# Performance work log

Hardware: AMD Instinct MI355X
Metric: run time of the kernel (lower is better)

## Reference

```python
import jax, jax.numpy as jnp
import numpy as np

X, U, AD, H = 32, 8, 24, 256
T, B = 128, 256
MIN_V, MAX_V = 0.01, 1.0
EPS = 1e-6


def setup_inputs() -> dict:
    key = jax.random.key(0)
    ks = jax.random.split(key, 10)
    s = lambda k, sh: jax.random.normal(k, sh, jnp.float32) * 0.05
    return {
        "u": jax.random.normal(ks[0], (T, B, U), jnp.float32),
        "a": jax.random.normal(ks[1], (T, B, AD), jnp.float32),
        "W1": s(ks[2], (H, X)), "b1": jnp.zeros((H,), jnp.float32),
        "W2": s(ks[3], (H, H)), "b2": jnp.zeros((H,), jnp.float32),
        "WA": s(ks[4], (X * X, H)), "bA": jnp.zeros((X * X,), jnp.float32),
        "WB": s(ks[5], (X * U, H)), "bB": jnp.zeros((X * U,), jnp.float32),
        "WC": s(ks[6], (AD * X, H)), "bC": jnp.zeros((AD * X,), jnp.float32),
        "Wnx": s(ks[7], (X, H)), "bnx": jnp.zeros((X,), jnp.float32),
        "Wna": s(ks[8], (AD, H)), "bna": jnp.zeros((AD,), jnp.float32),
        "alpha": jnp.array([0.01], jnp.float32),
    }


def _forward(u, a, W1, b1, W2, b2, WA, bA, WB, bB, WC, bC, Wnx, bnx, Wna, bna, alpha):
    eyeX = jnp.eye(X, dtype=u.dtype)
    eyeA = jnp.eye(AD, dtype=u.dtype)

    def dyn(x):
        # locally-linear dynamics heads; x: [B, X]
        h = jax.nn.relu(x @ W1.T + b1)
        h = jax.nn.relu(h @ W2.T + b2)
        b = x.shape[0]
        Am = eyeX + alpha[0] * (h @ WA.T + bA).reshape(b, X, X)
        Bm = (h @ WB.T + bB).reshape(b, X, U)
        Cm = (h @ WC.T + bC).reshape(b, AD, X)
        nx = MIN_V + (MAX_V - MIN_V) * jax.nn.sigmoid(h @ Wnx.T + bnx)
        na = MIN_V + (MAX_V - MIN_V) * jax.nn.sigmoid(h @ Wna.T + bna)
        return Am, Bm, Cm, nx, na

    def make_psd(P):
        return 0.5 * (P + jnp.swapaxes(P, -1, -2)) + EPS * eyeX

    def prior_step(mean, cov, u_t):
        Am, Bm, _, nx, _ = dyn(mean)
        nm = jnp.einsum('bij,bj->bi', Am, mean) + jnp.einsum('bij,bj->bi', Bm, u_t)
        nc = jnp.einsum('bij,bjk,blk->bil', Am, cov, Am) + nx[:, :, None] * eyeX
        return nm, make_psd(nc)

    def post_step(mean, cov, a_t):
        _, _, Cm, _, na = dyn(mean)
        S = jnp.einsum('bij,bjk,blk->bil', Cm, cov, Cm) + na[:, :, None] * eyeA
        Sp = jnp.linalg.pinv(S)
        G = jnp.einsum('bij,bkj,bkl->bil', cov, Cm, Sp)  # cov @ C^T @ pinv(S)
        innov = a_t - jnp.einsum('bij,bj->bi', Cm, mean)
        nm = mean + jnp.einsum('bij,bj->bi', G, innov)
        nc = cov - jnp.einsum('bij,bjk,bkl->bil', G, Cm, cov)
        return nm, make_psd(nc)

    pm0 = jnp.zeros((B, X), u.dtype)
    pc0 = jnp.broadcast_to(eyeX, (B, X, X))
    qm0, qc0 = post_step(pm0, pc0, a[0])

    def step(carry, inp):
        qm, qc = carry
        u_t, a_next = inp
        prm, prc = prior_step(qm, qc, u_t)
        nqm, nqc = post_step(prm, prc, a_next)
        return (nqm, nqc), (prm, prc, nqm, nqc)

    _, (prm, prc, qm, qc) = jax.lax.scan(step, (qm0, qc0), (u[:-1], a[1:]))
    prior_means = jnp.concatenate([pm0[None], prm], axis=0)
    prior_covs = jnp.concatenate([pc0[None], prc], axis=0)
    post_means = jnp.concatenate([qm0[None], qm], axis=0)
    post_covs = jnp.concatenate([qc0[None], qc], axis=0)
    return prior_means, prior_covs, post_means, post_covs


def reference(u, a, W1, b1, W2, b2, WA, bA, WB, bB, WC, bC, Wnx, bnx, Wna, bna, alpha):
    return _forward(u, a, W1, b1, W2, b2, WA, bA, WB, bB, WC, bC, Wnx, bnx, Wna, bna, alpha)
```

## Files before the change

kernel.cpp:

```cpp
#include <hip/hip_runtime.h>
#include <hip/hip_bf16.h>
#include <math.h>

typedef unsigned int uint32;
typedef _Float16 h2_t __attribute__((ext_vector_type(2)));

static constexpr int NX = 32;
static constexpr int NU = 8;
static constexpr int NA = 24;
static constexpr int NH = 256;
static constexpr int NT = 128;
static constexpr int NB = 256;
static constexpr float MINV = 0.01f, MAXV = 1.0f, EPSV = 1e-6f;

static constexpr int H1O = NX*NX + NX*NU + NX;
static constexpr int H1P = 1344;
static constexpr int H2O = NA*NX + NA;
static constexpr int H2P = 800;

static constexpr size_t OFF_W1 = 0;
static constexpr size_t OFF_W2 = 4096;
static constexpr size_t OFF_H1 = OFF_W2 + 32768;
static constexpr size_t OFF_H2 = OFF_H1 + 172032;
static constexpr size_t OFF_B1 = OFF_H2 + 102400;
static constexpr size_t OFF_B2 = OFF_B1 + 1344;

__global__ void pack_half_off(const float* __restrict__ src, uint32* __restrict__ dst,
                              int O, int K, int LDP, int off)
{
    int idx = blockIdx.x * blockDim.x + threadIdx.x;
    int K2 = K >> 1;
    if (idx >= O * K2) return;
    int kk = idx % K2;
    int o  = idx / K2;
    int k  = kk * 2;
    int k8 = k >> 3, q = (k >> 1) & 3;
    _Float16 a = (_Float16)src[o * K + k];
    _Float16 b = (_Float16)src[o * K + k + 1];
    uint32 val = (uint32)__builtin_bit_cast(unsigned short, a)
               | ((uint32)__builtin_bit_cast(unsigned short, b) << 16);
    dst[((size_t)k8 * LDP + off + o) * 4 + q] = val;
}

__global__ void pack_bias3(const float* __restrict__ s0, int n0,
                           const float* __restrict__ s1, int n1,
                           const float* __restrict__ s2, int n2,
                           float* __restrict__ dst)
{
    int i = blockIdx.x * blockDim.x + threadIdx.x;
    if (i < n0) dst[i] = s0[i];
    else if (i < n0 + n1) dst[i] = s1[i - n0];
    else if (i < n0 + n1 + n2) dst[i] = s2[i - n0 - n1];
}

__device__ __forceinline__ float dot2(uint32 w, uint32 x, float acc)
{
#if __has_builtin(__builtin_amdgcn_fdot2)
    return __builtin_amdgcn_fdot2(__builtin_bit_cast(h2_t, w),
                                  __builtin_bit_cast(h2_t, x), acc, false);
#else
    h2_t a = __builtin_bit_cast(h2_t, w), b = __builtin_bit_cast(h2_t, x);
    return acc + (float)a[0] * (float)b[0] + (float)a[1] * (float)b[1];
#endif
}

__device__ __forceinline__ float dot8(uint4 w, uint4 x, float acc)
{
    acc = dot2(w.x, x.x, acc);
    acc = dot2(w.y, x.y, acc);
    acc = dot2(w.z, x.z, acc);
    acc = dot2(w.w, x.w, acc);
    return acc;
}

__device__ __forceinline__ void tri_decode(int p, int& l, int& i)
{
    int lo = (int)((sqrtf(8.f * (float)p + 1.f) - 1.f) * 0.5f);
    while ((lo + 1) * (lo + 2) / 2 <= p) lo++;
    while (lo * (lo + 1) / 2 > p) lo--;
    l = lo;
    i = p - lo * (lo + 1) / 2;
}

__device__ __forceinline__ float sigm_scaled(float z)
{
    return MINV + (MAXV - MINV) / (1.f + expf(-z));
}

__device__ __forceinline__ unsigned short f2h(float v)
{
    _Float16 h = (_Float16)v;
    return __builtin_bit_cast(unsigned short, h);
}

__global__ __launch_bounds__(512) void kf_kernel(
    const float* __restrict__ u, const float* __restrict__ a,
    const uint32* __restrict__ wsu,
    const float* __restrict__ b1, const float* __restrict__ b2,
    const float* __restrict__ alpha_p,
    float* __restrict__ out)
{
    const int tid = threadIdx.x;
    const int b   = blockIdx.x;
    const float alpha = alpha_p[0];

    const uint4* W1h = (const uint4*)(wsu + OFF_W1);
    const uint4* W2h = (const uint4*)(wsu + OFF_W2);
    const uint4* H1h = (const uint4*)(wsu + OFF_H1);
    const uint4* H2h = (const uint4*)(wsu + OFF_H2);
    const float* BH1 = (const float*)(wsu + OFF_B1);
    const float* BH2 = (const float*)(wsu + OFF_B2);

    __shared__ alignas(16) uint32 s_h1h[NH / 2];
    __shared__ alignas(16) uint32 s_h2h[NH / 2];
    __shared__ alignas(16) uint32 s_qmh[NX / 2];
    __shared__ alignas(16) uint32 s_pmh[NX / 2];
    __shared__ float s_part[2][NH];
    __shared__ float s_Am[NX * NX];
    __shared__ float s_Bm[NX * NU];
    __shared__ float s_nx[NX];
    __shared__ float s_C[NA * NX];
    __shared__ float s_na[NA];
    __shared__ float s_qm[NX], s_qc[NX * NX];
    __shared__ float s_pm[NX], s_pc[NX * NX];
    __shared__ float s_T2[NX * NX];
    __shared__ float s_T1[NA * NX];
    __shared__ float s_S[NA * NA];
    __shared__ float s_Y[NA * NX];
    __shared__ float s_innov[NA];
    __shared__ float s_a[NA], s_u[NU];

    const size_t pmO = 0;
    const size_t pcO = (size_t)NT * NB * NX;
    const size_t qmO = pcO + (size_t)NT * NB * NX * NX;
    const size_t qcO = qmO + (size_t)NT * NB * NX;

    for (int t = 0; t < NT; ++t) {
        const size_t mIdx = (size_t)t * NB + b;

        if (t == 0) {
            if (tid < NX) s_pm[tid] = 0.f;
            if (tid < NX / 2) s_pmh[tid] = 0u;
            {
                int o = tid;           s_pc[o] = ((o >> 5) == (o & 31)) ? 1.f : 0.f;
                o = tid + 512;         s_pc[o] = ((o >> 5) == (o & 31)) ? 1.f : 0.f;
            }
            __syncthreads();
        } else {
            if (tid < NH) {
                const uint4* xh = (const uint4*)s_qmh;
                float acc = b1[tid];
                #pragma unroll
                for (int k8 = 0; k8 < 4; k8++)
                    acc = dot8(W1h[k8 * NH + tid], xh[k8], acc);
                float v = fmaxf(acc, 0.f);
                unsigned short us = f2h(v);
                int pi = __shfl_xor((int)us, 1);
                if ((tid & 1) == 0)
                    s_h1h[tid >> 1] = (uint32)us | ((uint32)pi << 16);
            } else {
                const size_t mPrev = (size_t)(t - 1) * NB + b;
                for (int s = tid - 256; s < NX + NX * NX; s += 256) {
                    if (s < NX)
                        __builtin_nontemporal_store(s_qm[s], out + qmO + mPrev * NX + s);
                    else
                        __builtin_nontemporal_store(s_qc[s - NX], out + qcO + mPrev * NX * NX + (s - NX));
                }
                if (tid - 256 < NU)
                    s_u[tid - 256] = u[((size_t)(t - 1) * NB + b) * NU + (tid - 256)];
            }
            __syncthreads();

            {
                int o = tid & 255, g = tid >> 8;
                const uint4* xh = (const uint4*)s_h1h;
                float acc = 0.f;
                #pragma unroll 4
                for (int k8 = g * 16; k8 < g * 16 + 16; k8++)
                    acc = dot8(W2h[k8 * NH + o], xh[k8], acc);
                s_part[g][o] = acc;
            }
            __syncthreads();

            if (tid < NH) {
                float v = fmaxf(s_part[0][tid] + s_part[1][tid] + b2[tid], 0.f);
                unsigned short us = f2h(v);
                int pi = __shfl_xor((int)us, 1);
                if ((tid & 1) == 0)
                    s_h2h[tid >> 1] = (uint32)us | ((uint32)pi << 16);
            }
            __syncthreads();

            {
                const uint4* xh = (const uint4*)s_h2h;
                int o0 = tid, o1 = tid + 512, o2 = tid + 1024;
                float a0 = BH1[o0], a1 = BH1[o1];
                float a2 = (tid < 320) ? BH1[o2] : 0.f;
                #pragma unroll 4
                for (int k8 = 0; k8 < 32; k8++) {
                    uint4 x = xh[k8];
                    a0 = dot8(H1h[k8 * H1P + o0], x, a0);
                    a1 = dot8(H1h[k8 * H1P + o1], x, a1);
                    if (tid < 320) a2 = dot8(H1h[k8 * H1P + o2], x, a2);
                }
                #pragma unroll
                for (int r = 0; r < 3; r++) {
                    int o = (r == 0) ? o0 : (r == 1) ? o1 : o2;
                    float acc = (r == 0) ? a0 : (r == 1) ? a1 : a2;
                    if (r == 2 && tid >= 320) break;
                    if (o < NX * NX) {
                        s_Am[o] = (((o >> 5) == (o & 31)) ? 1.f : 0.f) + alpha * acc;
                    } else if (o < NX * NX + NX * NU) {
                        s_Bm[o - NX * NX] = acc;
                    } else if (o < H1O) {
                        s_nx[o - (NX * NX + NX * NU)] = sigm_scaled(acc);
                    }
                }
            }
            __syncthreads();

            #pragma unroll
            for (int r = 0; r < 2; r++) {
                int o = tid + 512 * r, i = o >> 5, l = o & 31;
                float acc = 0.f;
                #pragma unroll
                for (int j = 0; j < NX; j++)
                    acc = fmaf(s_Am[i * NX + j], s_qc[j * NX + l], acc);
                s_T2[o] = acc;
            }
            if (tid < NX) {
                float acc = 0.f;
                #pragma unroll
                for (int j = 0; j < NX; j++) acc = fmaf(s_Am[tid * NX + j], s_qm[j], acc);
                #pragma unroll
                for (int j = 0; j < NU; j++) acc = fmaf(s_Bm[tid * NU + j], s_u[j], acc);
                s_pm[tid] = acc;
                unsigned short us = f2h(acc);
                int pi = __shfl_xor((int)us, 1);
                if ((tid & 1) == 0)
                    s_pmh[tid >> 1] = (uint32)us | ((uint32)pi << 16);
            }
            __syncthreads();

            for (int p = tid; p < NX * (NX + 1) / 2; p += 512) {
                int l, i; tri_decode(p, l, i);
                float a_il = 0.f, a_li = 0.f;
                #pragma unroll
                for (int j = 0; j < NX; j++) {
                    a_il = fmaf(s_T2[i * NX + j], s_Am[l * NX + j], a_il);
                    a_li = fmaf(s_T2[l * NX + j], s_Am[i * NX + j], a_li);
                }
                if (i == l) {
                    s_pc[i * NX + i] = a_il + s_nx[i] + EPSV;
                } else {
                    float v = 0.5f * (a_il + a_li);
                    s_pc[i * NX + l] = v;
                    s_pc[l * NX + i] = v;
                }
            }
            __syncthreads();
        }

        if (tid < NH) {
            const uint4* xh = (const uint4*)s_pmh;
            float acc = b1[tid];
            #pragma unroll
            for (int k8 = 0; k8 < 4; k8++)
                acc = dot8(W1h[k8 * NH + tid], xh[k8], acc);
            float v = fmaxf(acc, 0.f);
            unsigned short us = f2h(v);
            int pi = __shfl_xor((int)us, 1);
            if ((tid & 1) == 0)
                s_h1h[tid >> 1] = (uint32)us | ((uint32)pi << 16);
        } else {
            for (int s = tid - 256; s < NX + NX * NX; s += 256) {
                if (s < NX)
                    __builtin_nontemporal_store(s_pm[s], out + pmO + mIdx * NX + s);
                else
                    __builtin_nontemporal_store(s_pc[s - NX], out + pcO + mIdx * NX * NX + (s - NX));
            }
            if (tid - 256 < NA)
                s_a[tid - 256] = a[mIdx * NA + (tid - 256)];
        }
        __syncthreads();

        {
            int o = tid & 255, g = tid >> 8;
            const uint4* xh = (const uint4*)s_h1h;
            float acc = 0.f;
            #pragma unroll 4
            for (int k8 = g * 16; k8 < g * 16 + 16; k8++)
                acc = dot8(W2h[k8 * NH + o], xh[k8], acc);
            s_part[g][o] = acc;
        }
        __syncthreads();

        if (tid < NH) {
            float v = fmaxf(s_part[0][tid] + s_part[1][tid] + b2[tid], 0.f);
            unsigned short us = f2h(v);
            int pi = __shfl_xor((int)us, 1);
            if ((tid & 1) == 0)
                s_h2h[tid >> 1] = (uint32)us | ((uint32)pi << 16);
        }
        __syncthreads();

        {
            const uint4* xh = (const uint4*)s_h2h;
            int o0 = tid, o1 = tid + 512;
            float a0 = BH2[o0];
            float a1 = (tid < H2P - 512) ? BH2[o1] : 0.f;
            #pragma unroll 4
            for (int k8 = 0; k8 < 32; k8++) {
                uint4 x = xh[k8];
                a0 = dot8(H2h[k8 * H2P + o0], x, a0);
                if (tid < H2P - 512) a1 = dot8(H2h[k8 * H2P + o1], x, a1);
            }
            if (o0 < NA * NX) s_C[o0] = a0;
            else if (o0 < H2O) s_na[o0 - NA * NX] = sigm_scaled(a0);
            if (tid < H2P - 512) {
                if (o1 < NA * NX) s_C[o1] = a1;
                else if (o1 < H2O) s_na[o1 - NA * NX] = sigm_scaled(a1);
            }
        }
        __syncthreads();

        {
            int p = tid;
            if (p < NA * NX) {
                int i = p >> 5, l = p & 31;
                float acc = 0.f;
                #pragma unroll
                for (int k = 0; k < NX; k++)
                    acc = fmaf(s_C[i * NX + k], s_pc[k * NX + l], acc);
                s_T1[p] = acc;
            }
            int p2 = tid + 512;
            if (p2 < NA * NX) {
                int i = p2 >> 5, l = p2 & 31;
                float acc = 0.f;
                #pragma unroll
                for (int k = 0; k < NX; k++)
                    acc = fmaf(s_C[i * NX + k], s_pc[k * NX + l], acc);
                s_T1[p2] = acc;
            }
            if (tid >= 488) {
                int i = tid - 488;
                float acc = s_a[i];
                #pragma unroll
                for (int j = 0; j < NX; j++)
                    acc = fmaf(-s_C[i * NX + j], s_pm[j], acc);
                s_innov[i] = acc;
            }
        }
        __syncthreads();

        if (tid < NA * (NA + 1) / 2) {
            int l, i; tri_decode(tid, l, i);
            float acc = 0.f;
            #pragma unroll
            for (int j = 0; j < NX; j++)
                acc = fmaf(s_T1[i * NX + j], s_C[l * NX + j], acc);
            if (i == l) acc += s_na[i];
            s_S[i * NA + l] = acc;
            s_S[l * NA + i] = acc;
        }
        __syncthreads();

        if (tid < 64) {
            const int j = tid;
            float r[NA];
            #pragma unroll
            for (int i = 0; i < NA; i++) {
                float v = 0.f;
                if (j < NA) v = s_S[i * NA + j];
                else if (j < NA + NX) v = s_T1[i * NX + (j - NA)];
                r[i] = v;
            }
            #pragma unroll
            for (int k = 0; k < NA; k++) {
                float piv = __shfl(r[k], k);
                float ip = 1.0f / piv;
                r[k] *= ip;
                #pragma unroll
                for (int i = 0; i < NA; i++) {
                    if (i == k) continue;
                    float f = __shfl(r[i], k);
                    r[i] = fmaf(-f, r[k], r[i]);
                }
            }
            if (j >= NA && j < NA + NX) {
                #pragma unroll
                for (int i = 0; i < NA; i++) s_Y[i * NX + (j - NA)] = r[i];
            }
        }
        __syncthreads();

        if (tid < NX) {
            float acc = s_pm[tid];
            #pragma unroll
            for (int i = 0; i < NA; i++)
                acc = fmaf(s_Y[i * NX + tid], s_innov[i], acc);
            s_qm[tid] = acc;
            unsigned short us = f2h(acc);
            int pi = __shfl_xor((int)us, 1);
            if ((tid & 1) == 0)
                s_qmh[tid >> 1] = (uint32)us | ((uint32)pi << 16);
        }
        for (int p = tid; p < NX * (NX + 1) / 2; p += 512) {
            int l, i; tri_decode(p, l, i);
            float t_il = 0.f, t_li = 0.f;
            #pragma unroll
            for (int q = 0; q < NA; q++) {
                t_il = fmaf(s_Y[q * NX + i], s_T1[q * NX + l], t_il);
                t_li = fmaf(s_Y[q * NX + l], s_T1[q * NX + i], t_li);
            }
            if (i == l) {
                s_qc[i * NX + i] = s_pc[i * NX + i] - t_il + EPSV;
            } else {
                float v = 0.5f * ((s_pc[i * NX + l] - t_il) + (s_pc[l * NX + i] - t_li));
                s_qc[i * NX + l] = v;
                s_qc[l * NX + i] = v;
            }
        }
        __syncthreads();
    }

    {
        const size_t mLast = (size_t)(NT - 1) * NB + b;
        for (int s = tid; s < NX + NX * NX; s += 512) {
            if (s < NX)
                __builtin_nontemporal_store(s_qm[s], out + qmO + mLast * NX + s);
            else
                __builtin_nontemporal_store(s_qc[s - NX], out + qcO + mLast * NX * NX + (s - NX));
        }
    }
}

extern "C" void kernel_launch(void* const* d_in, const int* in_sizes, int n_in,
                              void* d_out, int out_size, void* d_ws, size_t ws_size,
                              hipStream_t stream)
{
    const float* u    = (const float*)d_in[0];
    const float* a    = (const float*)d_in[1];
    const float* W1   = (const float*)d_in[2];
    const float* b1   = (const float*)d_in[3];
    const float* W2   = (const float*)d_in[4];
    const float* b2   = (const float*)d_in[5];
    const float* WA   = (const float*)d_in[6];
    const float* bA   = (const float*)d_in[7];
    const float* WB   = (const float*)d_in[8];
    const float* bB   = (const float*)d_in[9];
    const float* WC   = (const float*)d_in[10];
    const float* bC   = (const float*)d_in[11];
    const float* Wnx  = (const float*)d_in[12];
    const float* bnx  = (const float*)d_in[13];
    const float* Wna  = (const float*)d_in[14];
    const float* bna  = (const float*)d_in[15];
    const float* alph = (const float*)d_in[16];

    uint32* wsu = (uint32*)d_ws;
    float* out = (float*)d_out;

    auto pk = [&](const float* src, int O, int K, size_t dst_off, int LDP, int off) {
        int n = O * (K / 2);
        pack_half_off<<<(n + 255) / 256, 256, 0, stream>>>(src, wsu + dst_off, O, K, LDP, off);
    };
    pk(W1,  NH,      NX, OFF_W1, NH,  0);
    pk(W2,  NH,      NH, OFF_W2, NH,  0);
    pk(WA,  NX * NX, NH, OFF_H1, H1P, 0);
    pk(WB,  NX * NU, NH, OFF_H1, H1P, NX * NX);
    pk(Wnx, NX,      NH, OFF_H1, H1P, NX * NX + NX * NU);
    pk(WC,  NA * NX, NH, OFF_H2, H2P, 0);
    pk(Wna, NA,      NH, OFF_H2, H2P, NA * NX);

    pack_bias3<<<(H1O + 255) / 256, 256, 0, stream>>>(bA, NX * NX, bB, NX * NU, bnx, NX,
                                                      (float*)(wsu + OFF_B1));
    pack_bias3<<<(H2O + 255) / 256, 256, 0, stream>>>(bC, NA * NX, bna, NA, nullptr, 0,
                                                      (float*)(wsu + OFF_B2));

    kf_kernel<<<NB, 512, 0, stream>>>(u, a, wsu, b1, b2, alph, out);
}
```

Baseline: 4.138 ms.

## Process two batch elements per block to reuse weight loads and pad shared matrices

Each block now runs the Kalman filter recurrence for two batch elements instead of one, so every fp16 weight vector loaded from global memory is used in two dot products. Shared-memory matrices are padded to a row stride of 33 to cut bank conflicts. The grid halves to 128 blocks, which on a 256-CU device leaves half the CUs idle and lengthens each block's per-step serial work. Shared-memory use also roughly doubles.

```diff
diff --git a/kernel.cpp b/kernel.cpp
--- a/kernel.cpp
+++ b/kernel.cpp
@@ -11,6 +11,7 @@
 static constexpr int NH = 256;
 static constexpr int NT = 128;
 static constexpr int NB = 256;
+static constexpr int NXP = NX + 1;
 static constexpr float MINV = 0.01f, MAXV = 1.0f, EPSV = 1e-6f;
 
 static constexpr int H1O = NX*NX + NX*NU + NX;
@@ -93,6 +94,18 @@
     return __builtin_bit_cast(unsigned short, h);
 }
 
+__device__ __forceinline__ void pack2_to(int tid, float v0, float v1,
+                                         uint32* d0, uint32* d1)
+{
+    unsigned short u0 = f2h(v0), u1 = f2h(v1);
+    int p0 = __shfl_xor((int)u0, 1);
+    int p1 = __shfl_xor((int)u1, 1);
+    if ((tid & 1) == 0) {
+        d0[tid >> 1] = (uint32)u0 | ((uint32)p0 << 16);
+        d1[tid >> 1] = (uint32)u1 | ((uint32)p1 << 16);
+    }
+}
+
 __global__ __launch_bounds__(512) void kf_kernel(
     const float* __restrict__ u, const float* __restrict__ a,
     const uint32* __restrict__ wsu,
@@ -101,7 +114,7 @@
     float* __restrict__ out)
 {
     const int tid = threadIdx.x;
-    const int b   = blockIdx.x;
+    const int b0  = blockIdx.x * 2;
     const float alpha = alpha_p[0];
 
     const uint4* W1h = (const uint4*)(wsu + OFF_W1);
@@ -111,24 +124,24 @@
     const float* BH1 = (const float*)(wsu + OFF_B1);
     const float* BH2 = (const float*)(wsu + OFF_B2);
 
-    __shared__ alignas(16) uint32 s_h1h[NH / 2];
-    __shared__ alignas(16) uint32 s_h2h[NH / 2];
-    __shared__ alignas(16) uint32 s_qmh[NX / 2];
-    __shared__ alignas(16) uint32 s_pmh[NX / 2];
-    __shared__ float s_part[2][NH];
-    __shared__ float s_Am[NX * NX];
-    __shared__ float s_Bm[NX * NU];
-    __shared__ float s_nx[NX];
-    __shared__ float s_C[NA * NX];
-    __shared__ float s_na[NA];
-    __shared__ float s_qm[NX], s_qc[NX * NX];
-    __shared__ float s_pm[NX], s_pc[NX * NX];
-    __shared__ float s_T2[NX * NX];
-    __shared__ float s_T1[NA * NX];
-    __shared__ float s_S[NA * NA];
-    __shared__ float s_Y[NA * NX];
-    __shared__ float s_innov[NA];
-    __shared__ float s_a[NA], s_u[NU];
+    __shared__ alignas(16) uint32 s_h1h[2][NH / 2];
+    __shared__ alignas(16) uint32 s_h2h[2][NH / 2];
+    __shared__ alignas(16) uint32 s_qmh[2][NX / 2];
+    __shared__ alignas(16) uint32 s_pmh[2][NX / 2];
+    __shared__ float s_part[2][2][NH];
+    __shared__ float s_Am[2][NX * NXP];
+    __shared__ float s_Bm[2][NX * NU];
+    __shared__ float s_nx[2][NX];
+    __shared__ float s_C[2][NA * NXP];
+    __shared__ float s_na[2][NA];
+    __shared__ float s_qm[2][NX], s_qc[2][NX * NXP];
+    __shared__ float s_pm[2][NX], s_pc[2][NX * NXP];
+    __shared__ float s_T2[2][NX * NXP];
+    __shared__ float s_T1[2][NA * NXP];
+    __shared__ float s_S[2][NA * NA];
+    __shared__ float s_Y[2][NA * NX];
+    __shared__ float s_innov[2][NA];
+    __shared__ float s_a[2][NA], s_u[2][NU];
 
     const size_t pmO = 0;
     const size_t pcO = (size_t)NT * NB * NX;
@@ -136,244 +149,292 @@
     const size_t qcO = qmO + (size_t)NT * NB * NX;
 
     for (int t = 0; t < NT; ++t) {
-        const size_t mIdx = (size_t)t * NB + b;
-
         if (t == 0) {
-            if (tid < NX) s_pm[tid] = 0.f;
-            if (tid < NX / 2) s_pmh[tid] = 0u;
-            {
-                int o = tid;           s_pc[o] = ((o >> 5) == (o & 31)) ? 1.f : 0.f;
-                o = tid + 512;         s_pc[o] = ((o >> 5) == (o & 31)) ? 1.f : 0.f;
+            if (tid < 64) s_pm[tid >> 5][tid & 31] = 0.f;
+            if (tid < 32) s_pmh[tid >> 4][tid & 15] = 0u;
+            #pragma unroll
+            for (int r = 0; r < 4; r++) {
+                int o = tid + 512 * r;
+                int e = o >> 10, oo = o & 1023, i = oo >> 5, l = oo & 31;
+                s_pc[e][i * NXP + l] = (i == l) ? 1.f : 0.f;
             }
             __syncthreads();
         } else {
             if (tid < NH) {
-                const uint4* xh = (const uint4*)s_qmh;
-                float acc = b1[tid];
-                #pragma unroll
-                for (int k8 = 0; k8 < 4; k8++)
-                    acc = dot8(W1h[k8 * NH + tid], xh[k8], acc);
-                float v = fmaxf(acc, 0.f);
-                unsigned short us = f2h(v);
-                int pi = __shfl_xor((int)us, 1);
-                if ((tid & 1) == 0)
-                    s_h1h[tid >> 1] = (uint32)us | ((uint32)pi << 16);
+                const uint4* x0 = (const uint4*)s_qmh[0];
+                const uint4* x1 = (const uint4*)s_qmh[1];
+                float a0 = b1[tid], a1e = b1[tid];
+                #pragma unroll
+                for (int k8 = 0; k8 < 4; k8++) {
+                    uint4 w = W1h[k8 * NH + tid];
+                    a0  = dot8(w, x0[k8], a0);
+                    a1e = dot8(w, x1[k8], a1e);
+                }
+                pack2_to(tid, fmaxf(a0, 0.f), fmaxf(a1e, 0.f), s_h1h[0], s_h1h[1]);
             } else {
-                const size_t mPrev = (size_t)(t - 1) * NB + b;
-                for (int s = tid - 256; s < NX + NX * NX; s += 256) {
-                    if (s < NX)
-                        __builtin_nontemporal_store(s_qm[s], out + qmO + mPrev * NX + s);
-                    else
-                        __builtin_nontemporal_store(s_qc[s - NX], out + qcO + mPrev * NX * NX + (s - NX));
-                }
-                if (tid - 256 < NU)
-                    s_u[tid - 256] = u[((size_t)(t - 1) * NB + b) * NU + (tid - 256)];
+                int s0 = tid - 256;
+                for (int s = s0; s < 2 * (NX + NX * NX); s += 256) {
+                    int e  = s >= (NX + NX * NX);
+                    int s2 = s - e * (NX + NX * NX);
+                    size_t mPrev = (size_t)(t - 1) * NB + b0 + e;
+                    if (s2 < NX)
+                        __builtin_nontemporal_store(s_qm[e][s2], out + qmO + mPrev * NX + s2);
+                    else {
+                        int o = s2 - NX, i = o >> 5, l = o & 31;
+                        __builtin_nontemporal_store(s_qc[e][i * NXP + l],
+                                                    out + qcO + mPrev * NX * NX + o);
+                    }
+                }
+                if (s0 < 2 * NU) {
+                    int e = s0 >> 3, j = s0 & 7;
+                    s_u[e][j] = u[((size_t)(t - 1) * NB + b0 + e) * NU + j];
+                }
             }
             __syncthreads();
 
             {
                 int o = tid & 255, g = tid >> 8;
-                const uint4* xh = (const uint4*)s_h1h;
-                float acc = 0.f;
+                const uint4* x0 = (const uint4*)s_h1h[0];
+                const uint4* x1 = (const uint4*)s_h1h[1];
+                float a0 = 0.f, a1e = 0.f;
                 #pragma unroll 4
-                for (int k8 = g * 16; k8 < g * 16 + 16; k8++)
-                    acc = dot8(W2h[k8 * NH + o], xh[k8], acc);
-                s_part[g][o] = acc;
+                for (int k8 = g * 16; k8 < g * 16 + 16; k8++) {
+                    uint4 w = W2h[k8 * NH + o];
+                    a0  = dot8(w, x0[k8], a0);
+                    a1e = dot8(w, x1[k8], a1e);
+                }
+                s_part[0][g][o] = a0;
+                s_part[1][g][o] = a1e;
             }
             __syncthreads();
 
             if (tid < NH) {
-                float v = fmaxf(s_part[0][tid] + s_part[1][tid] + b2[tid], 0.f);
-                unsigned short us = f2h(v);
-                int pi = __shfl_xor((int)us, 1);
-                if ((tid & 1) == 0)
-                    s_h2h[tid >> 1] = (uint32)us | ((uint32)pi << 16);
+                float v0 = fmaxf(s_part[0][0][tid] + s_part[0][1][tid] + b2[tid], 0.f);
+                float v1 = fmaxf(s_part[1][0][tid] + s_part[1][1][tid] + b2[tid], 0.f);
+                pack2_to(tid, v0, v1, s_h2h[0], s_h2h[1]);
             }
             __syncthreads();
 
             {
-                const uint4* xh = (const uint4*)s_h2h;
+                const uint4* x0 = (const uint4*)s_h2h[0];
+                const uint4* x1 = (const uint4*)s_h2h[1];
                 int o0 = tid, o1 = tid + 512, o2 = tid + 1024;
-                float a0 = BH1[o0], a1 = BH1[o1];
-                float a2 = (tid < 320) ? BH1[o2] : 0.f;
+                float bb0 = BH1[o0], bb1 = BH1[o1], bb2 = (tid < 320) ? BH1[o2] : 0.f;
+                float acc[2][3] = {{bb0, bb1, bb2}, {bb0, bb1, bb2}};
                 #pragma unroll 4
                 for (int k8 = 0; k8 < 32; k8++) {
-                    uint4 x = xh[k8];
-                    a0 = dot8(H1h[k8 * H1P + o0], x, a0);
-                    a1 = dot8(H1h[k8 * H1P + o1], x, a1);
-                    if (tid < 320) a2 = dot8(H1h[k8 * H1P + o2], x, a2);
-                }
-                #pragma unroll
-                for (int r = 0; r < 3; r++) {
-                    int o = (r == 0) ? o0 : (r == 1) ? o1 : o2;
-                    float acc = (r == 0) ? a0 : (r == 1) ? a1 : a2;
-                    if (r == 2 && tid >= 320) break;
-                    if (o < NX * NX) {
-                        s_Am[o] = (((o >> 5) == (o & 31)) ? 1.f : 0.f) + alpha * acc;
-                    } else if (o < NX * NX + NX * NU) {
-                        s_Bm[o - NX * NX] = acc;
-                    } else if (o < H1O) {
-                        s_nx[o - (NX * NX + NX * NU)] = sigm_scaled(acc);
+                    uint4 xa = x0[k8], xb = x1[k8];
+                    uint4 w0 = H1h[k8 * H1P + o0];
+                    acc[0][0] = dot8(w0, xa, acc[0][0]);
+                    acc[1][0] = dot8(w0, xb, acc[1][0]);
+                    uint4 w1 = H1h[k8 * H1P + o1];
+                    acc[0][1] = dot8(w1, xa, acc[0][1]);
+                    acc[1][1] = dot8(w1, xb, acc[1][1]);
+                    if (tid < 320) {
+                        uint4 w2 = H1h[k8 * H1P + o2];
+                        acc[0][2] = dot8(w2, xa, acc[0][2]);
+                        acc[1][2] = dot8(w2, xb, acc[1][2]);
                     }
                 }
-            }
-            __syncthreads();
-
-            #pragma unroll
-            for (int r = 0; r < 2; r++) {
-                int o = tid + 512 * r, i = o >> 5, l = o & 31;
+                #pragma unroll
+                for (int e = 0; e < 2; e++) {
+                    #pragma unroll
+                    for (int r = 0; r < 3; r++) {
+                        if (r == 2 && tid >= 320) break;
+                        int o = tid + 512 * r;
+                        float v = acc[e][r];
+                        if (o < NX * NX) {
+                            int i = o >> 5, l = o & 31;
+                            s_Am[e][i * NXP + l] = ((i == l) ? 1.f : 0.f) + alpha * v;
+                        } else if (o < NX * NX + NX * NU) {
+                            s_Bm[e][o - NX * NX] = v;
+                        } else if (o < H1O) {
+                            s_nx[e][o - (NX * NX + NX * NU)] = sigm_scaled(v);
+                        }
+                    }
+                }
+            }
+            __syncthreads();
+
+            #pragma unroll
+            for (int r = 0; r < 4; r++) {
+                int p = tid + 512 * r;
+                int e = p >> 10, o = p & 1023, i = o >> 5, l = o & 31;
                 float acc = 0.f;
                 #pragma unroll
                 for (int j = 0; j < NX; j++)
-                    acc = fmaf(s_Am[i * NX + j], s_qc[j * NX + l], acc);
-                s_T2[o] = acc;
-            }
-            if (tid < NX) {
+                    acc = fmaf(s_Am[e][i * NXP + j], s_qc[e][j * NXP + l], acc);
+                s_T2[e][i * NXP + l] = acc;
+            }
+            if (tid < 64) {
+                int e = tid >> 5, i = tid & 31;
                 float acc = 0.f;
                 #pragma unroll
-                for (int j = 0; j < NX; j++) acc = fmaf(s_Am[tid * NX + j], s_qm[j], acc);
-                #pragma unroll
-                for (int j = 0; j < NU; j++) acc = fmaf(s_Bm[tid * NU + j], s_u[j], acc);
-                s_pm[tid] = acc;
+                for (int j = 0; j < NX; j++) acc = fmaf(s_Am[e][i * NXP + j], s_qm[e][j], acc);
+                #pragma unroll
+                for (int j = 0; j < NU; j++) acc = fmaf(s_Bm[e][i * NU + j], s_u[e][j], acc);
+                s_pm[e][i] = acc;
                 unsigned short us = f2h(acc);
                 int pi = __shfl_xor((int)us, 1);
-                if ((tid & 1) == 0)
-                    s_pmh[tid >> 1] = (uint32)us | ((uint32)pi << 16);
-            }
-            __syncthreads();
-
-            for (int p = tid; p < NX * (NX + 1) / 2; p += 512) {
-                int l, i; tri_decode(p, l, i);
+                if ((tid & 1) == 0) s_pmh[e][i >> 1] = (uint32)us | ((uint32)pi << 16);
+            }
+            __syncthreads();
+
+            for (int p = tid; p < 2 * 528; p += 512) {
+                int e = p >= 528, pp = p - 528 * e;
+                int l, i; tri_decode(pp, l, i);
                 float a_il = 0.f, a_li = 0.f;
                 #pragma unroll
                 for (int j = 0; j < NX; j++) {
-                    a_il = fmaf(s_T2[i * NX + j], s_Am[l * NX + j], a_il);
-                    a_li = fmaf(s_T2[l * NX + j], s_Am[i * NX + j], a_li);
+                    a_il = fmaf(s_T2[e][i * NXP + j], s_Am[e][l * NXP + j], a_il);
+                    a_li = fmaf(s_T2[e][l * NXP + j], s_Am[e][i * NXP + j], a_li);
                 }
                 if (i == l) {
-                    s_pc[i * NX + i] = a_il + s_nx[i] + EPSV;
+                    s_pc[e][i * NXP + i] = a_il + s_nx[e][i] + EPSV;
                 } else {
                     float v = 0.5f * (a_il + a_li);
-                    s_pc[i * NX + l] = v;
-                    s_pc[l * NX + i] = v;
+                    s_pc[e][i * NXP + l] = v;
+                    s_pc[e][l * NXP + i] = v;
                 }
             }
             __syncthreads();
         }
 
         if (tid < NH) {
-            const uint4* xh = (const uint4*)s_pmh;
-            float acc = b1[tid];
-            #pragma unroll
-            for (int k8 = 0; k8 < 4; k8++)
-                acc = dot8(W1h[k8 * NH + tid], xh[k8], acc);
-            float v = fmaxf(acc, 0.f);
-            unsigned short us = f2h(v);
-            int pi = __shfl_xor((int)us, 1);
-            if ((tid & 1) == 0)
-                s_h1h[tid >> 1] = (uint32)us | ((uint32)pi << 16);
+            const uint4* x0 = (const uint4*)s_pmh[0];
+            const uint4* x1 = (const uint4*)s_pmh[1];
+            float a0 = b1[tid], a1e = b1[tid];
+            #pragma unroll
+            for (int k8 = 0; k8 < 4; k8++) {
+                uint4 w = W1h[k8 * NH + tid];
+                a0  = dot8(w, x0[k8], a0);
+                a1e = dot8(w, x1[k8], a1e);
+            }
+            pack2_to(tid, fmaxf(a0, 0.f), fmaxf(a1e, 0.f), s_h1h[0], s_h1h[1]);
         } else {
-            for (int s = tid - 256; s < NX + NX * NX; s += 256) {
-                if (s < NX)
-                    __builtin_nontemporal_store(s_pm[s], out + pmO + mIdx * NX + s);
-                else
-                    __builtin_nontemporal_store(s_pc[s - NX], out + pcO + mIdx * NX * NX + (s - NX));
-            }
-            if (tid - 256 < NA)
-                s_a[tid - 256] = a[mIdx * NA + (tid - 256)];
+            int s0 = tid - 256;
+            for (int s = s0; s < 2 * (NX + NX * NX); s += 256) {
+                int e  = s >= (NX + NX * NX);
+                int s2 = s - e * (NX + NX * NX);
+                size_t mIdx = (size_t)t * NB + b0 + e;
+                if (s2 < NX)
+                    __builtin_nontemporal_store(s_pm[e][s2], out + pmO + mIdx * NX + s2);
+                else {
+                    int o = s2 - NX, i = o >> 5, l = o & 31;
+                    __builtin_nontemporal_store(s_pc[e][i * NXP + l],
+                                                out + pcO + mIdx * NX * NX + o);
+                }
+            }
+            if (s0 < 2 * NA) {
+                int e = s0 >= NA, i = s0 - NA * e;
+                s_a[e][i] = a[((size_t)t * NB + b0 + e) * NA + i];
+            }
         }
         __syncthreads();
 
         {
             int o = tid & 255, g = tid >> 8;
-            const uint4* xh = (const uint4*)s_h1h;
-            float acc = 0.f;
+            const uint4* x0 = (const uint4*)s_h1h[0];
+            const uint4* x1 = (const uint4*)s_h1h[1];
+            float a0 = 0.f, a1e = 0.f;
             #pragma unroll 4
-            for (int k8 = g * 16; k8 < g * 16 + 16; k8++)
-                acc = dot8(W2h[k8 * NH + o], xh[k8], acc);
-            s_part[g][o] = acc;
+            for (int k8 = g * 16; k8 < g * 16 + 16; k8++) {
+                uint4 w = W2h[k8 * NH + o];
+                a0  = dot8(w, x0[k8], a0);
+                a1e = dot8(w, x1[k8], a1e);
+            }
+            s_part[0][g][o] = a0;
+            s_part[1][g][o] = a1e;
         }
         __syncthreads();
 
         if (tid < NH) {
-            float v = fmaxf(s_part[0][tid] + s_part[1][tid] + b2[tid], 0.f);
-            unsigned short us = f2h(v);
-            int pi = __shfl_xor((int)us, 1);
-            if ((tid & 1) == 0)
-                s_h2h[tid >> 1] = (uint32)us | ((uint32)pi << 16);
+            float v0 = fmaxf(s_part[0][0][tid] + s_part[0][1][tid] + b2[tid], 0.f);
+            float v1 = fmaxf(s_part[1][0][tid] + s_part[1][1][tid] + b2[tid], 0.f);
+            pack2_to(tid, v0, v1, s_h2h[0], s_h2h[1]);
         }
         __syncthreads();
 
         {
-            const uint4* xh = (const uint4*)s_h2h;
+            const uint4* x0 = (const uint4*)s_h2h[0];
+            const uint4* x1 = (const uint4*)s_h2h[1];
             int o0 = tid, o1 = tid + 512;
-            float a0 = BH2[o0];
-            float a1 = (tid < H2P - 512) ? BH2[o1] : 0.f;
+            float bb0 = BH2[o0], bb1 = (tid < H2P - 512) ? BH2[o1] : 0.f;
+            float acc[2][2] = {{bb0, bb1}, {bb0, bb1}};
             #pragma unroll 4
             for (int k8 = 0; k8 < 32; k8++) {
-                uint4 x = xh[k8];
-                a0 = dot8(H2h[k8 * H2P + o0], x, a0);
-                if (tid < H2P - 512) a1 = dot8(H2h[k8 * H2P + o1], x, a1);
-            }
-            if (o0 < NA * NX) s_C[o0] = a0;
-            else if (o0 < H2O) s_na[o0 - NA * NX] = sigm_scaled(a0);
-            if (tid < H2P - 512) {
-                if (o1 < NA * NX) s_C[o1] = a1;
-                else if (o1 < H2O) s_na[o1 - NA * NX] = sigm_scaled(a1);
-            }
-        }
-        __syncthreads();
-
-        {
-            int p = tid;
-            if (p < NA * NX) {
-                int i = p >> 5, l = p & 31;
-                float acc = 0.f;
-                #pragma unroll
-                for (int k = 0; k < NX; k++)
-                    acc = fmaf(s_C[i * NX + k], s_pc[k * NX + l], acc);
-                s_T1[p] = acc;
-            }
-            int p2 = tid + 512;
-            if (p2 < NA * NX) {
-                int i = p2 >> 5, l = p2 & 31;
-                float acc = 0.f;
-                #pragma unroll
-                for (int k = 0; k < NX; k++)
-                    acc = fmaf(s_C[i * NX + k], s_pc[k * NX + l], acc);
-                s_T1[p2] = acc;
-            }
-            if (tid >= 488) {
-                int i = tid - 488;
-                float acc = s_a[i];
-                #pragma unroll
-                for (int j = 0; j < NX; j++)
-                    acc = fmaf(-s_C[i * NX + j], s_pm[j], acc);
-                s_innov[i] = acc;
-            }
-        }
-        __syncthreads();
-
-        if (tid < NA * (NA + 1) / 2) {
-            int l, i; tri_decode(tid, l, i);
+                uint4 xa = x0[k8], xb = x1[k8];
+                uint4 w0 = H2h[k8 * H2P + o0];
+                acc[0][0] = dot8(w0, xa, acc[0][0]);
+                acc[1][0] = dot8(w0, xb, acc[1][0]);
+                if (tid < H2P - 512) {
+                    uint4 w1 = H2h[k8 * H2P + o1];
+                    acc[0][1] = dot8(w1, xa, acc[0][1]);
+                    acc[1][1] = dot8(w1, xb, acc[1][1]);
+                }
+            }
+            #pragma unroll
+            for (int e = 0; e < 2; e++) {
+                if (o0 < NA * NX) {
+                    int i = o0 >> 5, l = o0 & 31;
+                    s_C[e][i * NXP + l] = acc[e][0];
+                } else if (o0 < H2O) {
+                    s_na[e][o0 - NA * NX] = sigm_scaled(acc[e][0]);
+                }
+                if (tid < H2P - 512) {
+                    if (o1 < NA * NX) {
+                        int i = o1 >> 5, l = o1 & 31;
+                        s_C[e][i * NXP + l] = acc[e][1];
+                    } else if (o1 < H2O) {
+                        s_na[e][o1 - NA * NX] = sigm_scaled(acc[e][1]);
+                    }
+                }
+            }
+        }
+        __syncthreads();
+
+        #pragma unroll
+        for (int r = 0; r < 3; r++) {
+            int p = tid + 512 * r;
+            int e = p >= NA * NX, o = p - NA * NX * e, i = o >> 5, l = o & 31;
             float acc = 0.f;
             #pragma unroll
+            for (int k = 0; k < NX; k++)
+                acc = fmaf(s_C[e][i * NXP + k], s_pc[e][k * NXP + l], acc);
+            s_T1[e][i * NXP + l] = acc;
+        }
+        if (tid >= 464) {
+            int idx = tid - 464;
+            int e = idx >= NA, i = idx - NA * e;
+            float acc = s_a[e][i];
+            #pragma unroll
             for (int j = 0; j < NX; j++)
-                acc = fmaf(s_T1[i * NX + j], s_C[l * NX + j], acc);
-            if (i == l) acc += s_na[i];
-            s_S[i * NA + l] = acc;
-            s_S[l * NA + i] = acc;
-        }
-        __syncthreads();
-
-        if (tid < 64) {
-            const int j = tid;
+                acc = fmaf(-s_C[e][i * NXP + j], s_pm[e][j], acc);
+            s_innov[e][i] = acc;
+        }
+        __syncthreads();
+
+        for (int p = tid; p < 2 * 300; p += 512) {
+            int e = p >= 300, pp = p - 300 * e;
+            int l, i; tri_decode(pp, l, i);
+            float acc = 0.f;
+            #pragma unroll
+            for (int j = 0; j < NX; j++)
+                acc = fmaf(s_T1[e][i * NXP + j], s_C[e][l * NXP + j], acc);
+            if (i == l) acc += s_na[e][i];
+            s_S[e][i * NA + l] = acc;
+            s_S[e][l * NA + i] = acc;
+        }
+        __syncthreads();
+
+        if (tid < 128) {
+            int e = tid >> 6, j = tid & 63;
             float r[NA];
             #pragma unroll
             for (int i = 0; i < NA; i++) {
                 float v = 0.f;
-                if (j < NA) v = s_S[i * NA + j];
-                else if (j < NA + NX) v = s_T1[i * NX + (j - NA)];
+                if (j < NA) v = s_S[e][i * NA + j];
+                else if (j < NA + NX) v = s_T1[e][i * NXP + (j - NA)];
                 r[i] = v;
             }
             #pragma unroll
@@ -390,48 +451,52 @@
             }
             if (j >= NA && j < NA + NX) {
                 #pragma unroll
-                for (int i = 0; i < NA; i++) s_Y[i * NX + (j - NA)] = r[i];
-            }
-        }
-        __syncthreads();
-
-        if (tid < NX) {
-            float acc = s_pm[tid];
-            #pragma unroll
-            for (int i = 0; i < NA; i++)
-                acc = fmaf(s_Y[i * NX + tid], s_innov[i], acc);
-            s_qm[tid] = acc;
+                for (int i = 0; i < NA; i++) s_Y[e][i * NX + (j - NA)] = r[i];
+            }
+        }
+        __syncthreads();
+
+        if (tid < 64) {
+            int e = tid >> 5, i = tid & 31;
+            float acc = s_pm[e][i];
+            #pragma unroll
+            for (int q = 0; q < NA; q++)
+                acc = fmaf(s_Y[e][q * NX + i], s_innov[e][q], acc);
+            s_qm[e][i] = acc;
             unsigned short us = f2h(acc);
             int pi = __shfl_xor((int)us, 1);
-            if ((tid & 1) == 0)
-                s_qmh[tid >> 1] = (uint32)us | ((uint32)pi << 16);
-        }
-        for (int p = tid; p < NX * (NX + 1) / 2; p += 512) {
-            int l, i; tri_decode(p, l, i);
+            if ((tid & 1) == 0) s_qmh[e][i >> 1] = (uint32)us | ((uint32)pi << 16);
+        }
+        for (int p = tid; p < 2 * 528; p += 512) {
+            int e = p >= 528, pp = p - 528 * e;
+            int l, i; tri_decode(pp, l, i);
             float t_il = 0.f, t_li = 0.f;
             #pragma unroll
             for (int q = 0; q < NA; q++) {
-                t_il = fmaf(s_Y[q * NX + i], s_T1[q * NX + l], t_il);
-                t_li = fmaf(s_Y[q * NX + l], s_T1[q * NX + i], t_li);
+                t_il = fmaf(s_Y[e][q * NX + i], s_T1[e][q * NXP + l], t_il);
+                t_li = fmaf(s_Y[e][q * NX + l], s_T1[e][q * NXP + i], t_li);
             }
             if (i == l) {
-                s_qc[i * NX + i] = s_pc[i * NX + i] - t_il + EPSV;
+                s_qc[e][i * NXP + i] = s_pc[e][i * NXP + i] - t_il + EPSV;
             } else {
-                float v = 0.5f * ((s_pc[i * NX + l] - t_il) + (s_pc[l * NX + i] - t_li));
-                s_qc[i * NX + l] = v;
-                s_qc[l * NX + i] = v;
+                float v = 0.5f * ((s_pc[e][i * NXP + l] - t_il) + (s_pc[e][l * NXP + i] - t_li));
+                s_qc[e][i * NXP + l] = v;
+                s_qc[e][l * NXP + i] = v;
             }
         }
         __syncthreads();
     }
 
-    {
-        const size_t mLast = (size_t)(NT - 1) * NB + b;
-        for (int s = tid; s < NX + NX * NX; s += 512) {
-            if (s < NX)
-                __builtin_nontemporal_store(s_qm[s], out + qmO + mLast * NX + s);
-            else
-                __builtin_nontemporal_store(s_qc[s - NX], out + qcO + mLast * NX * NX + (s - NX));
+    for (int s = tid; s < 2 * (NX + NX * NX); s += 512) {
+        int e  = s >= (NX + NX * NX);
+        int s2 = s - e * (NX + NX * NX);
+        size_t mLast = (size_t)(NT - 1) * NB + b0 + e;
+        if (s2 < NX)
+            __builtin_nontemporal_store(s_qm[e][s2], out + qmO + mLast * NX + s2);
+        else {
+            int o = s2 - NX, i = o >> 5, l = o & 31;
+            __builtin_nontemporal_store(s_qc[e][i * NXP + l],
+                                        out + qcO + mLast * NX * NX + o);
         }
     }
 }
@@ -478,5 +543,5 @@
     pack_bias3<<<(H2O + 255) / 256, 256, 0, stream>>>(bC, NA * NX, bna, NA, nullptr, 0,
                                                       (float*)(wsu + OFF_B2));
 
-    kf_kernel<<<NB, 512, 0, stream>>>(u, a, wsu, b1, b2, alph, out);
-}
+    kf_kernel<<<NB / 2, 512, 0, stream>>>(u, a, wsu, b1, b2, alph, out);
+}
```

New measurement: 5.688 ms. +37.5%, slower.

## Double block size to 1024 threads and pad shared matrices to stride 33

Applied to the files above, without the earlier changes.

Launches the per-batch Kalman filter block with 1024 threads instead of 512, so each thread computes one output per matmul stage and the W2 reduction is split four ways instead of two. The shared-memory covariance, A, C and temporary matrices are padded to a row stride of 33 to avoid LDS bank conflicts in the row-wise dot products. In exchange, register pressure per thread rises under the larger launch bound, and there are more idle lanes in the small stages.

```diff
diff --git a/kernel.cpp b/kernel.cpp
--- a/kernel.cpp
+++ b/kernel.cpp
@@ -11,6 +11,7 @@
 static constexpr int NH = 256;
 static constexpr int NT = 128;
 static constexpr int NB = 256;
+static constexpr int NXP = NX + 1;
 static constexpr float MINV = 0.01f, MAXV = 1.0f, EPSV = 1e-6f;
 
 static constexpr int H1O = NX*NX + NX*NU + NX;
@@ -93,7 +94,15 @@
     return __builtin_bit_cast(unsigned short, h);
 }
 
-__global__ __launch_bounds__(512) void kf_kernel(
+__device__ __forceinline__ void pack1_to(int tid, float v, uint32* d)
+{
+    unsigned short us = f2h(v);
+    int pi = __shfl_xor((int)us, 1);
+    if ((tid & 1) == 0)
+        d[tid >> 1] = (uint32)us | ((uint32)pi << 16);
+}
+
+__global__ __launch_bounds__(1024) void kf_kernel(
     const float* __restrict__ u, const float* __restrict__ a,
     const uint32* __restrict__ wsu,
     const float* __restrict__ b1, const float* __restrict__ b2,
@@ -115,16 +124,16 @@
     __shared__ alignas(16) uint32 s_h2h[NH / 2];
     __shared__ alignas(16) uint32 s_qmh[NX / 2];
     __shared__ alignas(16) uint32 s_pmh[NX / 2];
-    __shared__ float s_part[2][NH];
-    __shared__ float s_Am[NX * NX];
+    __shared__ float s_part[4][NH];
+    __shared__ float s_Am[NX * NXP];
     __shared__ float s_Bm[NX * NU];
     __shared__ float s_nx[NX];
-    __shared__ float s_C[NA * NX];
+    __shared__ float s_C[NA * NXP];
     __shared__ float s_na[NA];
-    __shared__ float s_qm[NX], s_qc[NX * NX];
-    __shared__ float s_pm[NX], s_pc[NX * NX];
-    __shared__ float s_T2[NX * NX];
-    __shared__ float s_T1[NA * NX];
+    __shared__ float s_qm[NX], s_qc[NX * NXP];
+    __shared__ float s_pm[NX], s_pc[NX * NXP];
+    __shared__ float s_T2[NX * NXP];
+    __shared__ float s_T1[NA * NXP];
     __shared__ float s_S[NA * NA];
     __shared__ float s_Y[NA * NX];
     __shared__ float s_innov[NA];
@@ -141,9 +150,9 @@
         if (t == 0) {
             if (tid < NX) s_pm[tid] = 0.f;
             if (tid < NX / 2) s_pmh[tid] = 0u;
-            {
-                int o = tid;           s_pc[o] = ((o >> 5) == (o & 31)) ? 1.f : 0.f;
-                o = tid + 512;         s_pc[o] = ((o >> 5) == (o & 31)) ? 1.f : 0.f;
+            if (tid < NX * NX) {
+                int i = tid >> 5, l = tid & 31;
+                s_pc[i * NXP + l] = (i == l) ? 1.f : 0.f;
             }
             __syncthreads();
         } else {
@@ -153,18 +162,17 @@
                 #pragma unroll
                 for (int k8 = 0; k8 < 4; k8++)
                     acc = dot8(W1h[k8 * NH + tid], xh[k8], acc);
-                float v = fmaxf(acc, 0.f);
-                unsigned short us = f2h(v);
-                int pi = __shfl_xor((int)us, 1);
-                if ((tid & 1) == 0)
-                    s_h1h[tid >> 1] = (uint32)us | ((uint32)pi << 16);
+                pack1_to(tid, fmaxf(acc, 0.f), s_h1h);
             } else {
                 const size_t mPrev = (size_t)(t - 1) * NB + b;
-                for (int s = tid - 256; s < NX + NX * NX; s += 256) {
+                for (int s = tid - 256; s < NX + NX * NX; s += 768) {
                     if (s < NX)
                         __builtin_nontemporal_store(s_qm[s], out + qmO + mPrev * NX + s);
-                    else
-                        __builtin_nontemporal_store(s_qc[s - NX], out + qcO + mPrev * NX * NX + (s - NX));
+                    else {
+                        int o = s - NX, i = o >> 5, l = o & 31;
+                        __builtin_nontemporal_store(s_qc[i * NXP + l],
+                                                    out + qcO + mPrev * NX * NX + o);
+                    }
                 }
                 if (tid - 256 < NU)
                     s_u[tid - 256] = u[((size_t)(t - 1) * NB + b) * NU + (tid - 256)];
@@ -175,87 +183,75 @@
                 int o = tid & 255, g = tid >> 8;
                 const uint4* xh = (const uint4*)s_h1h;
                 float acc = 0.f;
-                #pragma unroll 4
-                for (int k8 = g * 16; k8 < g * 16 + 16; k8++)
+                #pragma unroll 8
+                for (int k8 = g * 8; k8 < g * 8 + 8; k8++)
                     acc = dot8(W2h[k8 * NH + o], xh[k8], acc);
                 s_part[g][o] = acc;
             }
             __syncthreads();
 
             if (tid < NH) {
-                float v = fmaxf(s_part[0][tid] + s_part[1][tid] + b2[tid], 0.f);
-                unsigned short us = f2h(v);
-                int pi = __shfl_xor((int)us, 1);
-                if ((tid & 1) == 0)
-                    s_h2h[tid >> 1] = (uint32)us | ((uint32)pi << 16);
+                float v = fmaxf(s_part[0][tid] + s_part[1][tid] +
+                                s_part[2][tid] + s_part[3][tid] + b2[tid], 0.f);
+                pack1_to(tid, v, s_h2h);
             }
             __syncthreads();
 
             {
                 const uint4* xh = (const uint4*)s_h2h;
-                int o0 = tid, o1 = tid + 512, o2 = tid + 1024;
-                float a0 = BH1[o0], a1 = BH1[o1];
-                float a2 = (tid < 320) ? BH1[o2] : 0.f;
-                #pragma unroll 4
+                int o0 = tid, o1 = tid + 1024;
+                float a0 = BH1[o0];
+                float a1 = (tid < H1O - 1024) ? BH1[o1] : 0.f;
+                #pragma unroll 8
                 for (int k8 = 0; k8 < 32; k8++) {
                     uint4 x = xh[k8];
                     a0 = dot8(H1h[k8 * H1P + o0], x, a0);
-                    a1 = dot8(H1h[k8 * H1P + o1], x, a1);
-                    if (tid < 320) a2 = dot8(H1h[k8 * H1P + o2], x, a2);
-                }
-                #pragma unroll
-                for (int r = 0; r < 3; r++) {
-                    int o = (r == 0) ? o0 : (r == 1) ? o1 : o2;
-                    float acc = (r == 0) ? a0 : (r == 1) ? a1 : a2;
-                    if (r == 2 && tid >= 320) break;
-                    if (o < NX * NX) {
-                        s_Am[o] = (((o >> 5) == (o & 31)) ? 1.f : 0.f) + alpha * acc;
-                    } else if (o < NX * NX + NX * NU) {
-                        s_Bm[o - NX * NX] = acc;
-                    } else if (o < H1O) {
-                        s_nx[o - (NX * NX + NX * NU)] = sigm_scaled(acc);
-                    }
-                }
-            }
-            __syncthreads();
-
-            #pragma unroll
-            for (int r = 0; r < 2; r++) {
-                int o = tid + 512 * r, i = o >> 5, l = o & 31;
+                    if (tid < H1O - 1024) a1 = dot8(H1h[k8 * H1P + o1], x, a1);
+                }
+                {
+                    int i = o0 >> 5, l = o0 & 31;
+                    s_Am[i * NXP + l] = ((i == l) ? 1.f : 0.f) + alpha * a0;
+                }
+                if (tid < H1O - 1024) {
+                    if (o1 < NX * NX + NX * NU) s_Bm[o1 - NX * NX] = a1;
+                    else s_nx[o1 - (NX * NX + NX * NU)] = sigm_scaled(a1);
+                }
+            }
+            __syncthreads();
+
+            {
+                int i = tid >> 5, l = tid & 31;
                 float acc = 0.f;
                 #pragma unroll
                 for (int j = 0; j < NX; j++)
-                    acc = fmaf(s_Am[i * NX + j], s_qc[j * NX + l], acc);
-                s_T2[o] = acc;
+                    acc = fmaf(s_Am[i * NXP + j], s_qc[j * NXP + l], acc);
+                s_T2[i * NXP + l] = acc;
             }
             if (tid < NX) {
                 float acc = 0.f;
                 #pragma unroll
-                for (int j = 0; j < NX; j++) acc = fmaf(s_Am[tid * NX + j], s_qm[j], acc);
+                for (int j = 0; j < NX; j++) acc = fmaf(s_Am[tid * NXP + j], s_qm[j], acc);
                 #pragma unroll
                 for (int j = 0; j < NU; j++) acc = fmaf(s_Bm[tid * NU + j], s_u[j], acc);
                 s_pm[tid] = acc;
-                unsigned short us = f2h(acc);
-                int pi = __shfl_xor((int)us, 1);
-                if ((tid & 1) == 0)
-                    s_pmh[tid >> 1] = (uint32)us | ((uint32)pi << 16);
-            }
-            __syncthreads();
-
-            for (int p = tid; p < NX * (NX + 1) / 2; p += 512) {
-                int l, i; tri_decode(p, l, i);
+                pack1_to(tid, acc, s_pmh);
+            }
+            __syncthreads();
+
+            if (tid < NX * (NX + 1) / 2) {
+                int l, i; tri_decode(tid, l, i);
                 float a_il = 0.f, a_li = 0.f;
                 #pragma unroll
                 for (int j = 0; j < NX; j++) {
-                    a_il = fmaf(s_T2[i * NX + j], s_Am[l * NX + j], a_il);
-                    a_li = fmaf(s_T2[l * NX + j], s_Am[i * NX + j], a_li);
+                    a_il = fmaf(s_T2[i * NXP + j], s_Am[l * NXP + j], a_il);
+                    a_li = fmaf(s_T2[l * NXP + j], s_Am[i * NXP + j], a_li);
                 }
                 if (i == l) {
-                    s_pc[i * NX + i] = a_il + s_nx[i] + EPSV;
+                    s_pc[i * NXP + i] = a_il + s_nx[i] + EPSV;
                 } else {
                     float v = 0.5f * (a_il + a_li);
-                    s_pc[i * NX + l] = v;
-                    s_pc[l * NX + i] = v;
+                    s_pc[i * NXP + l] = v;
+                    s_pc[l * NXP + i] = v;
                 }
             }
             __syncthreads();
@@ -267,17 +263,16 @@
             #pragma unroll
             for (int k8 = 0; k8 < 4; k8++)
                 acc = dot8(W1h[k8 * NH + tid], xh[k8], acc);
-            float v = fmaxf(acc, 0.f);
-            unsigned short us = f2h(v);
-            int pi = __shfl_xor((int)us, 1);
-            if ((tid & 1) == 0)
-                s_h1h[tid >> 1] = (uint32)us | ((uint32)pi << 16);
+            pack1_to(tid, fmaxf(acc, 0.f), s_h1h);
         } else {
-            for (int s = tid - 256; s < NX + NX * NX; s += 256) {
+            for (int s = tid - 256; s < NX + NX * NX; s += 768) {
                 if (s < NX)
                     __builtin_nontemporal_store(s_pm[s], out + pmO + mIdx * NX + s);
-                else
-                    __builtin_nontemporal_store(s_pc[s - NX], out + pcO + mIdx * NX * NX + (s - NX));
+                else {
+                    int o = s - NX, i = o >> 5, l = o & 31;
+                    __builtin_nontemporal_store(s_pc[i * NXP + l],
+                                                out + pcO + mIdx * NX * NX + o);
+                }
             }
             if (tid - 256 < NA)
                 s_a[tid - 256] = a[mIdx * NA + (tid - 256)];
@@ -288,69 +283,50 @@
             int o = tid & 255, g = tid >> 8;
             const uint4* xh = (const uint4*)s_h1h;
             float acc = 0.f;
-            #pragma unroll 4
-            for (int k8 = g * 16; k8 < g * 16 + 16; k8++)
+            #pragma unroll 8
+            for (int k8 = g * 8; k8 < g * 8 + 8; k8++)
                 acc = dot8(W2h[k8 * NH + o], xh[k8], acc);
             s_part[g][o] = acc;
         }
         __syncthreads();
 
         if (tid < NH) {
-            float v = fmaxf(s_part[0][tid] + s_part[1][tid] + b2[tid], 0.f);
-            unsigned short us = f2h(v);
-            int pi = __shfl_xor((int)us, 1);
-            if ((tid & 1) == 0)
-                s_h2h[tid >> 1] = (uint32)us | ((uint32)pi << 16);
-        }
-        __syncthreads();
-
-        {
+            float v = fmaxf(s_part[0][tid] + s_part[1][tid] +
+                            s_part[2][tid] + s_part[3][tid] + b2[tid], 0.f);
+            pack1_to(tid, v, s_h2h);
+        }
+        __syncthreads();
+
+        if (tid < H2P) {
             const uint4* xh = (const uint4*)s_h2h;
-            int o0 = tid, o1 = tid + 512;
-            float a0 = BH2[o0];
-            float a1 = (tid < H2P - 512) ? BH2[o1] : 0.f;
-            #pragma unroll 4
-            for (int k8 = 0; k8 < 32; k8++) {
-                uint4 x = xh[k8];
-                a0 = dot8(H2h[k8 * H2P + o0], x, a0);
-                if (tid < H2P - 512) a1 = dot8(H2h[k8 * H2P + o1], x, a1);
-            }
-            if (o0 < NA * NX) s_C[o0] = a0;
-            else if (o0 < H2O) s_na[o0 - NA * NX] = sigm_scaled(a0);
-            if (tid < H2P - 512) {
-                if (o1 < NA * NX) s_C[o1] = a1;
-                else if (o1 < H2O) s_na[o1 - NA * NX] = sigm_scaled(a1);
-            }
-        }
-        __syncthreads();
-
-        {
-            int p = tid;
-            if (p < NA * NX) {
-                int i = p >> 5, l = p & 31;
-                float acc = 0.f;
-                #pragma unroll
-                for (int k = 0; k < NX; k++)
-                    acc = fmaf(s_C[i * NX + k], s_pc[k * NX + l], acc);
-                s_T1[p] = acc;
-            }
-            int p2 = tid + 512;
-            if (p2 < NA * NX) {
-                int i = p2 >> 5, l = p2 & 31;
-                float acc = 0.f;
-                #pragma unroll
-                for (int k = 0; k < NX; k++)
-                    acc = fmaf(s_C[i * NX + k], s_pc[k * NX + l], acc);
-                s_T1[p2] = acc;
-            }
-            if (tid >= 488) {
-                int i = tid - 488;
-                float acc = s_a[i];
-                #pragma unroll
-                for (int j = 0; j < NX; j++)
-                    acc = fmaf(-s_C[i * NX + j], s_pm[j], acc);
-                s_innov[i] = acc;
-            }
+            float acc = BH2[tid];
+            #pragma unroll 8
+            for (int k8 = 0; k8 < 32; k8++)
+                acc = dot8(H2h[k8 * H2P + tid], xh[k8], acc);
+            if (tid < NA * NX) {
+                int i = tid >> 5, l = tid & 31;
+                s_C[i * NXP + l] = acc;
+            } else if (tid < H2O) {
+                s_na[tid - NA * NX] = sigm_scaled(acc);
+            }
+        }
+        __syncthreads();
+
+        if (tid < NA * NX) {
+            int i = tid >> 5, l = tid & 31;
+            float acc = 0.f;
+            #pragma unroll
+            for (int k = 0; k < NX; k++)
+                acc = fmaf(s_C[i * NXP + k], s_pc[k * NXP + l], acc);
+            s_T1[i * NXP + l] = acc;
+        }
+        if (tid >= 1000) {
+            int i = tid - 1000;
+            float acc = s_a[i];
+            #pragma unroll
+            for (int j = 0; j < NX; j++)
+                acc = fmaf(-s_C[i * NXP + j], s_pm[j], acc);
+            s_innov[i] = acc;
         }
         __syncthreads();
 
@@ -359,7 +335,7 @@
             float acc = 0.f;
             #pragma unroll
             for (int j = 0; j < NX; j++)
-                acc = fmaf(s_T1[i * NX + j], s_C[l * NX + j], acc);
+                acc = fmaf(s_T1[i * NXP + j], s_C[l * NXP + j], acc);
             if (i == l) acc += s_na[i];
             s_S[i * NA + l] = acc;
             s_S[l * NA + i] = acc;
@@ -373,7 +349,7 @@
             for (int i = 0; i < NA; i++) {
                 float v = 0.f;
                 if (j < NA) v = s_S[i * NA + j];
-                else if (j < NA + NX) v = s_T1[i * NX + (j - NA)];
+                else if (j < NA + NX) v = s_T1[i * NXP + (j - NA)];
                 r[i] = v;
             }
             #pragma unroll
@@ -401,25 +377,22 @@
             for (int i = 0; i < NA; i++)
                 acc = fmaf(s_Y[i * NX + tid], s_innov[i], acc);
             s_qm[tid] = acc;
-            unsigned short us = f2h(acc);
-            int pi = __shfl_xor((int)us, 1);
-            if ((tid & 1) == 0)
-                s_qmh[tid >> 1] = (uint32)us | ((uint32)pi << 16);
-        }
-        for (int p = tid; p < NX * (NX + 1) / 2; p += 512) {
-            int l, i; tri_decode(p, l, i);
+            pack1_to(tid, acc, s_qmh);
+        }
+        if (tid < NX * (NX + 1) / 2) {
+            int l, i; tri_decode(tid, l, i);
             float t_il = 0.f, t_li = 0.f;
             #pragma unroll
             for (int q = 0; q < NA; q++) {
-                t_il = fmaf(s_Y[q * NX + i], s_T1[q * NX + l], t_il);
-                t_li = fmaf(s_Y[q * NX + l], s_T1[q * NX + i], t_li);
+                t_il = fmaf(s_Y[q * NX + i], s_T1[q * NXP + l], t_il);
+                t_li = fmaf(s_Y[q * NX + l], s_T1[q * NXP + i], t_li);
             }
             if (i == l) {
-                s_qc[i * NX + i] = s_pc[i * NX + i] - t_il + EPSV;
+                s_qc[i * NXP + i] = s_pc[i * NXP + i] - t_il + EPSV;
             } else {
-                float v = 0.5f * ((s_pc[i * NX + l] - t_il) + (s_pc[l * NX + i] - t_li));
-                s_qc[i * NX + l] = v;
-                s_qc[l * NX + i] = v;
+                float v = 0.5f * ((s_pc[i * NXP + l] - t_il) + (s_pc[l * NXP + i] - t_li));
+                s_qc[i * NXP + l] = v;
+                s_qc[l * NXP + i] = v;
             }
         }
         __syncthreads();
@@ -427,11 +400,14 @@
 
     {
         const size_t mLast = (size_t)(NT - 1) * NB + b;
-        for (int s = tid; s < NX + NX * NX; s += 512) {
+        for (int s = tid; s < NX + NX * NX; s += 1024) {
             if (s < NX)
                 __builtin_nontemporal_store(s_qm[s], out + qmO + mLast * NX + s);
-            else
-                __builtin_nontemporal_store(s_qc[s - NX], out + qcO + mLast * NX * NX + (s - NX));
+            else {
+                int o = s - NX, i = o >> 5, l = o & 31;
+                __builtin_nontemporal_store(s_qc[i * NXP + l],
+                                            out + qcO + mLast * NX * NX + o);
+            }
         }
     }
 }
@@ -478,5 +454,5 @@
     pack_bias3<<<(H2O + 255) / 256, 256, 0, stream>>>(bC, NA * NX, bna, NA, nullptr, 0,
                                                       (float*)(wsu + OFF_B2));
 
-    kf_kernel<<<NB, 512, 0, stream>>>(u, a, wsu, b1, b2, alph, out);
-}
+    kf_kernel<<<NB, 1024, 0, stream>>>(u, a, wsu, b1, b2, alph, out);
+}
```

Result: slower. 5.802 ms (+40.2%).
